# Optimization experiments

Measured on AMD Instinct MI355X. Metric: run time of the kernel, lower is better.

The kernel has to match this reference:

```python
import jax, jax.numpy as jnp
import numpy as np

HIDDEN = 150
EMBED = 300
OUT = 5
VOCAB = 100000
DEPTH = 13                      # complete binary tree
N = 2 ** DEPTH - 1              # 8191 nodes
L = 2 ** (DEPTH - 1)            # 4096 leaves
SCALE = 0.01


def _build_tree():
    # heap layout: node i internal iff i < N - L; children 2i+1, 2i+2
    words = np.full(N, -1, dtype=np.int64)
    rng = np.random.RandomState(0)
    words[N - L:] = rng.randint(0, VOCAB, size=L)
    lchs = np.zeros(N, dtype=np.int64)
    rchs = np.zeros(N, dtype=np.int64)
    internal = np.arange(N - L)
    lchs[internal] = 2 * internal + 1
    rchs[internal] = 2 * internal + 2
    scores = rng.randint(0, OUT, size=N).astype(np.int64)
    return scores, words, lchs, rchs


def setup_inputs() -> dict:
    key = jax.random.key(0)
    ks = jax.random.split(key, 24)
    p = lambda i, shp: jax.random.normal(ks[i], shp, dtype=jnp.float32) * SCALE
    scores, words, lchs, rchs = _build_tree()
    return {
        "Wi": p(0, (HIDDEN, EMBED)), "bi": p(1, (HIDDEN,)),
        "Wo": p(2, (HIDDEN, EMBED)), "bo": p(3, (HIDDEN,)),
        "Wu": p(4, (HIDDEN, EMBED)), "bu": p(5, (HIDDEN,)),
        "U0i": p(6, (HIDDEN, HIDDEN)), "U1i": p(7, (HIDDEN, HIDDEN)), "bbi": p(8, (HIDDEN,)),
        "U00f": p(9, (HIDDEN, HIDDEN)), "U01f": p(10, (HIDDEN, HIDDEN)),
        "U10f": p(11, (HIDDEN, HIDDEN)), "U11f": p(12, (HIDDEN, HIDDEN)), "bbf": p(13, (HIDDEN,)),
        "U0o": p(14, (HIDDEN, HIDDEN)), "U1o": p(15, (HIDDEN, HIDDEN)), "bbo": p(16, (HIDDEN,)),
        "U0u": p(17, (HIDDEN, HIDDEN)), "U1u": p(18, (HIDDEN, HIDDEN)), "bbu": p(19, (HIDDEN,)),
        "Why": p(20, (OUT, HIDDEN)), "by": p(21, (OUT,)),
        "word_embedding": jax.random.normal(ks[22], (VOCAB, EMBED), dtype=jnp.float32),
        "scores": jnp.asarray(scores), "words": jnp.asarray(words),
        "lchs": jnp.asarray(lchs), "rchs": jnp.asarray(rchs),
    }


def _tree_loss(Wi, bi, Wo, bo, Wu, bu, U0i, U1i, bbi, U00f, U01f, U10f, U11f,
               bbf, U0o, U1o, bbo, U0u, U1u, bbu, Why, by, word_embedding,
               scores, words, lchs, rchs):
    n = scores.shape[0]
    depth = int(np.log2(n + 1))
    leaf_start = 2 ** (depth - 1) - 1

    H_all = jnp.zeros((n, HIDDEN), dtype=Wi.dtype)
    C_all = jnp.zeros((n, HIDDEN), dtype=Wi.dtype)

    # leaf level (batched): cell = sigmoid(Wi e + bi) * tanh(Wu e + bu)
    emb = word_embedding[words[leaf_start:]]              # [L, 300]
    ig = jax.nn.sigmoid(emb @ Wi.T + bi)
    og = jax.nn.sigmoid(emb @ Wo.T + bo)
    uv = jnp.tanh(emb @ Wu.T + bu)
    c = ig * uv
    h = og * jnp.tanh(c)
    H_all = H_all.at[leaf_start:].set(h)
    C_all = C_all.at[leaf_start:].set(c)

    # internal levels, children-before-parents (level-wise batched Tree-LSTM)
    for d in range(depth - 2, -1, -1):
        s, e = 2 ** d - 1, 2 ** (d + 1) - 1
        li, ri = lchs[s:e], rchs[s:e]
        lh, rh = H_all[li], H_all[ri]
        lc, rc = C_all[li], C_all[ri]
        ig = jax.nn.sigmoid(lh @ U0i.T + rh @ U1i.T + bbi)
        fl = jax.nn.sigmoid(lh @ U00f.T + rh @ U01f.T + bbf)
        fr = jax.nn.sigmoid(lh @ U10f.T + rh @ U11f.T + bbf)
        og = jax.nn.sigmoid(lh @ U0o.T + rh @ U1o.T + bbo)
        uv = jnp.tanh(lh @ U0u.T + rh @ U1u.T + bbu)
        c = ig * uv + fl * lc + fr * rc
        h = og * jnp.tanh(c)
        H_all = H_all.at[s:e].set(h)
        C_all = C_all.at[s:e].set(c)

    # per-node NLL loss, summed over all nodes
    logits = H_all @ Why.T + by                            # [N, 5]
    logp = jax.nn.log_softmax(logits, axis=1)
    return -jnp.sum(logp[jnp.arange(n), scores])


def reference(Wi, bi, Wo, bo, Wu, bu, U0i, U1i, bbi, U00f, U01f, U10f, U11f,
              bbf, U0o, U1o, bbo, U0u, U1u, bbu, Why, by, word_embedding,
              scores, words, lchs, rchs):
    return _tree_loss(Wi, bi, Wo, bo, Wu, bu, U0i, U1i, bbi, U00f, U01f,
                      U10f, U11f, bbf, U0o, U1o, bbo, U0u, U1u, bbu, Why, by,
                      word_embedding, scores, words, lchs, rchs)
```

## Files before the change

kernel.cpp:

```cpp
#include <hip/hip_runtime.h>
#include <math.h>

#define HID 150
#define EMB 300
#define NOUT 5
#define NNODES 8191
#define NLEAF 4096
#define LEAF_START 4095
#define HSTR 152
#define UCOLS 768
#define WCOLS 452

constexpr int LOSS_BLOCKS = 64;

__device__ __forceinline__ float sigmoidf_(float x) { return 1.0f / (1.0f + __expf(-x)); }

__global__ __launch_bounds__(256) void prep_kernel(
    const float* __restrict__ Wi, const float* __restrict__ Wo, const float* __restrict__ Wu,
    const float* __restrict__ U0i, const float* __restrict__ U1i,
    const float* __restrict__ U00f, const float* __restrict__ U01f,
    const float* __restrict__ U10f, const float* __restrict__ U11f,
    const float* __restrict__ U0o, const float* __restrict__ U1o,
    const float* __restrict__ U0u, const float* __restrict__ U1u,
    float* __restrict__ Wt2, float* __restrict__ Ut3, float* __restrict__ Ut4)
{
    int idx = blockIdx.x * 256 + threadIdx.x;
    if (idx < EMB * WCOLS) {
        int e = idx / WCOLS, j = idx - e * WCOLS;
        float v = 0.f;
        if (j < 450) {
            const float* W; int h;
            if (j < 150)      { W = Wi; h = j; }
            else if (j < 300) { W = Wo; h = j - 150; }
            else              { W = Wu; h = j - 300; }
            v = W[h * EMB + e];
        }
        Wt2[idx] = v;
    }
    if (idx < EMB * UCOLS) {
        int e = idx / UCOLS, j = idx - e * UCOLS;
        const float* U0[5] = {U0i, U00f, U10f, U0o, U0u};
        const float* U1[5] = {U1i, U01f, U11f, U1o, U1u};
        {
            int hc = j >> 8, cw = j & 255;
            float v = 0.f;
            if (cw < 250) {
                int g = cw / 50, hp = cw - g * 50, h = hc * 50 + hp;
                v = (e < 150) ? U0[g][h * HID + e] : U1[g][h * HID + (e - 150)];
            }
            Ut3[idx] = v;
        }
        {
            int hc = j >> 7, cw = j & 127;
            float v = 0.f;
            if (cw < 125) {
                int g = cw / 25, hp = cw - g * 25, h = hc * 25 + hp;
                v = (e < 150) ? U0[g][h * HID + e] : U1[g][h * HID + (e - 150)];
            }
            Ut4[idx] = v;
        }
    }
}

__global__ __launch_bounds__(256) void leaf_v3(
    const float* __restrict__ Wt2,
    const float* __restrict__ bi, const float* __restrict__ bo, const float* __restrict__ bu,
    const float* __restrict__ emb, const int* __restrict__ words,
    float* __restrict__ H, float* __restrict__ C)
{
    constexpr int NB = 8;
    __shared__ __align__(16) float Xs[EMB * NB];
    __shared__ __align__(16) float Gs[2][NB][WCOLS];
    const int tid = threadIdx.x;
    const int leaf0 = LEAF_START + blockIdx.x * NB;

    for (int m = 0; m < NB; ++m) {
        const float* src = emb + (long)words[leaf0 + m] * EMB;
        for (int e = tid; e < EMB; e += 256) Xs[e * NB + m] = src[e];
    }
    __syncthreads();

    {
        const int half = tid >> 7;
        const int c = tid & 127;
        if (c < 113) {
            float acc[NB][4];
#pragma unroll
            for (int m = 0; m < NB; ++m)
#pragma unroll
                for (int q = 0; q < 4; ++q) acc[m][q] = 0.f;

            const int kbase = half * 150;
            const float* wp = Wt2 + (long)kbase * WCOLS + c * 4;
            const float* xp = Xs + kbase * NB;
#pragma unroll 4
            for (int k = 0; k < 150; ++k) {
                float4 w = *(const float4*)(wp + (long)k * WCOLS);
                float4 xa = *(const float4*)(xp + k * NB);
                float4 xb = *(const float4*)(xp + k * NB + 4);
                float x[NB] = {xa.x, xa.y, xa.z, xa.w, xb.x, xb.y, xb.z, xb.w};
#pragma unroll
                for (int m = 0; m < NB; ++m) {
                    acc[m][0] = fmaf(x[m], w.x, acc[m][0]);
                    acc[m][1] = fmaf(x[m], w.y, acc[m][1]);
                    acc[m][2] = fmaf(x[m], w.z, acc[m][2]);
                    acc[m][3] = fmaf(x[m], w.w, acc[m][3]);
                }
            }
#pragma unroll
            for (int m = 0; m < NB; ++m)
                *(float4*)&Gs[half][m][c * 4] = make_float4(acc[m][0], acc[m][1], acc[m][2], acc[m][3]);
        }
    }
    __syncthreads();

    for (int p = tid; p < NB * HID; p += 256) {
        int m = p / HID, h = p - m * HID;
        float gi = Gs[0][m][h]       + Gs[1][m][h];
        float go = Gs[0][m][150 + h] + Gs[1][m][150 + h];
        float gu = Gs[0][m][300 + h] + Gs[1][m][300 + h];
        float ig = sigmoidf_(gi + bi[h]);
        float og = sigmoidf_(go + bo[h]);
        float uv = tanhf(gu + bu[h]);
        float cc = ig * uv;
        float hh = og * tanhf(cc);
        long node = leaf0 + m;
        H[node * HSTR + h] = hh;
        C[node * HSTR + h] = cc;
    }
}

template<int NB>
__global__ __launch_bounds__(512) void level_h3(
    const float* __restrict__ Ut3,
    const float* __restrict__ bbi, const float* __restrict__ bbf,
    const float* __restrict__ bbo, const float* __restrict__ bbu,
    const int* __restrict__ lchs, const int* __restrict__ rchs,
    float* __restrict__ H, float* __restrict__ C, int s)
{
    __shared__ __align__(16) float Xs[EMB * NB];
    __shared__ __align__(16) float Gs[4][NB][256];
    __shared__ int lidx[NB], ridx[NB];
    const int tid = threadIdx.x;
    const int grp = blockIdx.x / 3, hc = blockIdx.x % 3;
    const int node0 = s + grp * NB;

    if (tid < NB) {
        lidx[tid] = lchs[node0 + tid];
        ridx[tid] = rchs[node0 + tid];
    }
    __syncthreads();

    for (int m = 0; m < NB; ++m) {
        const float* hl = H + (long)lidx[m] * HSTR;
        const float* hr = H + (long)ridx[m] * HSTR;
        for (int e = tid; e < EMB; e += 512)
            Xs[e * NB + m] = (e < HID) ? hl[e] : hr[e - HID];
    }
    __syncthreads();

    {
        const int kq = tid >> 7, c2 = tid & 127;
        float acc[NB][2];
#pragma unroll
        for (int m = 0; m < NB; ++m) { acc[m][0] = 0.f; acc[m][1] = 0.f; }

        const float* wp = Ut3 + (long)(kq * 75) * UCOLS + hc * 256 + 2 * c2;
        const float* xp = Xs + (kq * 75) * NB;
#pragma unroll 5
        for (int k = 0; k < 75; ++k) {
            float2 w = *(const float2*)(wp + (long)k * UCOLS);
            float x[NB];
            if constexpr (NB == 8) {
                float4 a = *(const float4*)(xp + k * 8);
                float4 b = *(const float4*)(xp + k * 8 + 4);
                x[0]=a.x; x[1]=a.y; x[2]=a.z; x[3]=a.w;
                x[4]=b.x; x[5]=b.y; x[6]=b.z; x[7]=b.w;
            } else if constexpr (NB == 4) {
                float4 a = *(const float4*)(xp + k * 4);
                x[0]=a.x; x[1]=a.y; x[2]=a.z; x[3]=a.w;
            } else if constexpr (NB == 2) {
                float2 a = *(const float2*)(xp + k * 2);
                x[0]=a.x; x[1]=a.y;
            } else {
                x[0] = xp[k];
            }
#pragma unroll
            for (int m = 0; m < NB; ++m) {
                acc[m][0] = fmaf(x[m], w.x, acc[m][0]);
                acc[m][1] = fmaf(x[m], w.y, acc[m][1]);
            }
        }
#pragma unroll
        for (int m = 0; m < NB; ++m)
            *(float2*)&Gs[kq][m][2 * c2] = make_float2(acc[m][0], acc[m][1]);
    }
    __syncthreads();

    for (int p = tid; p < NB * 50; p += 512) {
        int m = p / 50, hp = p - m * 50, h = hc * 50 + hp;
        float gi  = Gs[0][m][hp]       + Gs[1][m][hp]       + Gs[2][m][hp]       + Gs[3][m][hp];
        float gf0 = Gs[0][m][50 + hp]  + Gs[1][m][50 + hp]  + Gs[2][m][50 + hp]  + Gs[3][m][50 + hp];
        float gf1 = Gs[0][m][100 + hp] + Gs[1][m][100 + hp] + Gs[2][m][100 + hp] + Gs[3][m][100 + hp];
        float go  = Gs[0][m][150 + hp] + Gs[1][m][150 + hp] + Gs[2][m][150 + hp] + Gs[3][m][150 + hp];
        float gu  = Gs[0][m][200 + hp] + Gs[1][m][200 + hp] + Gs[2][m][200 + hp] + Gs[3][m][200 + hp];
        float ig = sigmoidf_(gi + bbi[h]);
        float fl = sigmoidf_(gf0 + bbf[h]);
        float fr = sigmoidf_(gf1 + bbf[h]);
        float og = sigmoidf_(go + bbo[h]);
        float uv = tanhf(gu + bbu[h]);
        float lc = C[(long)lidx[m] * HSTR + h];
        float rc = C[(long)ridx[m] * HSTR + h];
        float cc = ig * uv + fl * lc + fr * rc;
        float hh = og * tanhf(cc);
        long node = node0 + m;
        H[node * HSTR + h] = hh;
        C[node * HSTR + h] = cc;
    }
}

__global__ __launch_bounds__(512) void level_h6(
    const float* __restrict__ Ut4,
    const float* __restrict__ bbi, const float* __restrict__ bbf,
    const float* __restrict__ bbo, const float* __restrict__ bbu,
    const int* __restrict__ lchs, const int* __restrict__ rchs,
    float* __restrict__ H, float* __restrict__ C, int s)
{
    __shared__ __align__(16) float Xs[EMB];
    __shared__ __align__(16) float Gs[4][128];
    __shared__ int lr[2];
    const int tid = threadIdx.x;
    const int grp = blockIdx.x / 6, hc = blockIdx.x % 6;
    const int node = s + grp;

    if (tid < 2) lr[tid] = tid ? rchs[node] : lchs[node];
    __syncthreads();
    if (tid < EMB)
        Xs[tid] = (tid < HID) ? H[(long)lr[0] * HSTR + tid] : H[(long)lr[1] * HSTR + (tid - HID)];
    __syncthreads();

    {
        const int kq = tid >> 7, c = tid & 127;
        float acc = 0.f;
        const float* wp = Ut4 + (long)(kq * 75) * UCOLS + hc * 128 + c;
        const float* xp = Xs + kq * 75;
#pragma unroll 15
        for (int k = 0; k < 75; ++k)
            acc = fmaf(xp[k], wp[(long)k * UCOLS], acc);
        Gs[kq][c] = acc;
    }
    __syncthreads();

    if (tid < 25) {
        int hp = tid, h = hc * 25 + hp;
        float gi  = Gs[0][hp]       + Gs[1][hp]       + Gs[2][hp]       + Gs[3][hp];
        float gf0 = Gs[0][25 + hp]  + Gs[1][25 + hp]  + Gs[2][25 + hp]  + Gs[3][25 + hp];
        float gf1 = Gs[0][50 + hp]  + Gs[1][50 + hp]  + Gs[2][50 + hp]  + Gs[3][50 + hp];
        float go  = Gs[0][75 + hp]  + Gs[1][75 + hp]  + Gs[2][75 + hp]  + Gs[3][75 + hp];
        float gu  = Gs[0][100 + hp] + Gs[1][100 + hp] + Gs[2][100 + hp] + Gs[3][100 + hp];
        float ig = sigmoidf_(gi + bbi[h]);
        float fl = sigmoidf_(gf0 + bbf[h]);
        float fr = sigmoidf_(gf1 + bbf[h]);
        float og = sigmoidf_(go + bbo[h]);
        float uv = tanhf(gu + bbu[h]);
        float lc = C[(long)lr[0] * HSTR + h];
        float rc = C[(long)lr[1] * HSTR + h];
        float cc = ig * uv + fl * lc + fr * rc;
        float hh = og * tanhf(cc);
        H[(long)node * HSTR + h] = hh;
        C[(long)node * HSTR + h] = cc;
    }
}

__global__ __launch_bounds__(256) void loss_kernel(
    const float* __restrict__ H, const float* __restrict__ Why,
    const float* __restrict__ by, const int* __restrict__ scores,
    float* __restrict__ partials)
{
    __shared__ __align__(16) float Wys[NOUT][HSTR];
    __shared__ float bys[NOUT];
    __shared__ float red[256];
    int tid = threadIdx.x;
    for (int i = tid; i < NOUT * HID; i += 256) {
        int g = i / HID, k = i - g * HID;
        Wys[g][k] = Why[g * HID + k];
    }
    if (tid < NOUT) bys[tid] = by[tid];
    __syncthreads();

    float local = 0.f;
    for (int n = blockIdx.x * 256 + tid; n < NNODES; n += gridDim.x * 256) {
        const float* hr = H + (long)n * HSTR;
        float l0 = bys[0], l1 = bys[1], l2 = bys[2], l3 = bys[3], l4 = bys[4];
        for (int k = 0; k < 148; k += 4) {
            float4 hv = *(const float4*)(hr + k);
            float4 w0 = *(const float4*)&Wys[0][k];
            float4 w1 = *(const float4*)&Wys[1][k];
            float4 w2 = *(const float4*)&Wys[2][k];
            float4 w3 = *(const float4*)&Wys[3][k];
            float4 w4 = *(const float4*)&Wys[4][k];
            l0 += hv.x*w0.x + hv.y*w0.y + hv.z*w0.z + hv.w*w0.w;
            l1 += hv.x*w1.x + hv.y*w1.y + hv.z*w1.z + hv.w*w1.w;
            l2 += hv.x*w2.x + hv.y*w2.y + hv.z*w2.z + hv.w*w2.w;
            l3 += hv.x*w3.x + hv.y*w3.y + hv.z*w3.z + hv.w*w3.w;
            l4 += hv.x*w4.x + hv.y*w4.y + hv.z*w4.z + hv.w*w4.w;
        }
        for (int k = 148; k < HID; ++k) {
            float hv = hr[k];
            l0 += hv * Wys[0][k]; l1 += hv * Wys[1][k]; l2 += hv * Wys[2][k];
            l3 += hv * Wys[3][k]; l4 += hv * Wys[4][k];
        }
        float mx = fmaxf(fmaxf(fmaxf(l0, l1), fmaxf(l2, l3)), l4);
        float se = __expf(l0 - mx) + __expf(l1 - mx) + __expf(l2 - mx) +
                   __expf(l3 - mx) + __expf(l4 - mx);
        float lse = mx + __logf(se);
        int sc = scores[n];
        float lsc = (sc == 0) ? l0 : (sc == 1) ? l1 : (sc == 2) ? l2 : (sc == 3) ? l3 : l4;
        local += lse - lsc;
    }
    red[tid] = local;
    __syncthreads();
    for (int st = 128; st > 0; st >>= 1) {
        if (tid < st) red[tid] += red[tid + st];
        __syncthreads();
    }
    if (tid == 0) partials[blockIdx.x] = red[0];
}

__global__ void loss_final(const float* __restrict__ partials, float* __restrict__ out, int nparts)
{
    if (threadIdx.x == 0 && blockIdx.x == 0) {
        float s = 0.f;
        for (int i = 0; i < nparts; ++i) s += partials[i];
        out[0] = s;
    }
}

extern "C" void kernel_launch(void* const* d_in, const int* in_sizes, int n_in,
                              void* d_out, int out_size, void* d_ws, size_t ws_size,
                              hipStream_t stream)
{
    const float* Wi   = (const float*)d_in[0];
    const float* bi   = (const float*)d_in[1];
    const float* Wo   = (const float*)d_in[2];
    const float* bo   = (const float*)d_in[3];
    const float* Wu   = (const float*)d_in[4];
    const float* bu   = (const float*)d_in[5];
    const float* U0i  = (const float*)d_in[6];
    const float* U1i  = (const float*)d_in[7];
    const float* bbi  = (const float*)d_in[8];
    const float* U00f = (const float*)d_in[9];
    const float* U01f = (const float*)d_in[10];
    const float* U10f = (const float*)d_in[11];
    const float* U11f = (const float*)d_in[12];
    const float* bbf  = (const float*)d_in[13];
    const float* U0o  = (const float*)d_in[14];
    const float* U1o  = (const float*)d_in[15];
    const float* bbo  = (const float*)d_in[16];
    const float* U0u  = (const float*)d_in[17];
    const float* U1u  = (const float*)d_in[18];
    const float* bbu  = (const float*)d_in[19];
    const float* Why  = (const float*)d_in[20];
    const float* by   = (const float*)d_in[21];
    const float* emb  = (const float*)d_in[22];
    const int* scores = (const int*)d_in[23];
    const int* words  = (const int*)d_in[24];
    const int* lchs   = (const int*)d_in[25];
    const int* rchs   = (const int*)d_in[26];

    float* ws = (float*)d_ws;
    float* Wt2 = ws;
    float* Ut3 = Wt2 + EMB * WCOLS;
    float* Ut4 = Ut3 + EMB * UCOLS;
    float* H   = Ut4 + EMB * UCOLS;
    float* C   = H + (long)NNODES * HSTR;
    float* partials = C + (long)NNODES * HSTR;
    float* out = (float*)d_out;

    hipLaunchKernelGGL(prep_kernel, dim3(900), dim3(256), 0, stream,
                       Wi, Wo, Wu, U0i, U1i, U00f, U01f, U10f, U11f,
                       U0o, U1o, U0u, U1u, Wt2, Ut3, Ut4);

    hipLaunchKernelGGL(leaf_v3, dim3(NLEAF / 8), dim3(256), 0, stream,
                       Wt2, bi, bo, bu, emb, words, H, C);

    for (int d = 11; d >= 0; --d) {
        int s = (1 << d) - 1, count = 1 << d;
        if (d >= 10) {
            hipLaunchKernelGGL(HIP_KERNEL_NAME(level_h3<8>), dim3((count / 8) * 3), dim3(512), 0, stream,
                               Ut3, bbi, bbf, bbo, bbu, lchs, rchs, H, C, s);
        } else if (d == 9) {
            hipLaunchKernelGGL(HIP_KERNEL_NAME(level_h3<4>), dim3((count / 4) * 3), dim3(512), 0, stream,
                               Ut3, bbi, bbf, bbo, bbu, lchs, rchs, H, C, s);
        } else if (d == 8) {
            hipLaunchKernelGGL(HIP_KERNEL_NAME(level_h3<2>), dim3((count / 2) * 3), dim3(512), 0, stream,
                               Ut3, bbi, bbf, bbo, bbu, lchs, rchs, H, C, s);
        } else if (d == 7) {
            hipLaunchKernelGGL(HIP_KERNEL_NAME(level_h3<1>), dim3(count * 3), dim3(512), 0, stream,
                               Ut3, bbi, bbf, bbo, bbu, lchs, rchs, H, C, s);
        } else {
            hipLaunchKernelGGL(level_h6, dim3(count * 6), dim3(512), 0, stream,
                               Ut4, bbi, bbf, bbo, bbu, lchs, rchs, H, C, s);
        }
    }

    hipLaunchKernelGGL(loss_kernel, dim3(LOSS_BLOCKS), dim3(256), 0, stream,
                       H, Why, by, scores, partials);
    hipLaunchKernelGGL(loss_final, dim3(1), dim3(64), 0, stream,
                       partials, out, LOSS_BLOCKS);
}
```

Measured before the change: 369.8 us.

## Batch more nodes per block in leaf and wide tree levels

The leaf kernel now processes 16 leaves per 512-thread block, and a new level kernel handles 16 nodes per block for the two widest internal levels. Smaller levels shift to larger per-block node batches, and the gather of child states and embeddings is flattened across all threads. The aim is more reuse of each weight load across nodes, cutting weight traffic per node, at the cost of fewer blocks, more registers and more shared memory per block, which can reduce occupancy on the narrower levels.

```diff
diff --git a/kernel.cpp b/kernel.cpp
--- a/kernel.cpp
+++ b/kernel.cpp
@@ -62,59 +62,62 @@
     }
 }
 
-__global__ __launch_bounds__(256) void leaf_v3(
+__global__ __launch_bounds__(512) void leaf_v4(
     const float* __restrict__ Wt2,
     const float* __restrict__ bi, const float* __restrict__ bo, const float* __restrict__ bu,
     const float* __restrict__ emb, const int* __restrict__ words,
     float* __restrict__ H, float* __restrict__ C)
 {
-    constexpr int NB = 8;
+    constexpr int NB = 16;
     __shared__ __align__(16) float Xs[EMB * NB];
     __shared__ __align__(16) float Gs[2][NB][WCOLS];
+    __shared__ int wq[NB];
     const int tid = threadIdx.x;
     const int leaf0 = LEAF_START + blockIdx.x * NB;
 
-    for (int m = 0; m < NB; ++m) {
-        const float* src = emb + (long)words[leaf0 + m] * EMB;
-        for (int e = tid; e < EMB; e += 256) Xs[e * NB + m] = src[e];
+    if (tid < NB) wq[tid] = words[leaf0 + tid];
+    __syncthreads();
+
+    for (int p = tid; p < NB * EMB; p += 512) {
+        int m = p / EMB, e = p - m * EMB;
+        Xs[e * NB + m] = emb[(long)wq[m] * EMB + e];
     }
     __syncthreads();
 
     {
-        const int half = tid >> 7;
-        const int c = tid & 127;
-        if (c < 113) {
-            float acc[NB][4];
-#pragma unroll
-            for (int m = 0; m < NB; ++m)
-#pragma unroll
-                for (int q = 0; q < 4; ++q) acc[m][q] = 0.f;
-
-            const int kbase = half * 150;
-            const float* wp = Wt2 + (long)kbase * WCOLS + c * 4;
+        const int kq = tid >> 8;
+        const int c = tid & 255;
+        if (c < 226) {
+            float acc[NB][2];
+#pragma unroll
+            for (int m = 0; m < NB; ++m) { acc[m][0] = 0.f; acc[m][1] = 0.f; }
+
+            const int kbase = kq * 150;
+            const float* wp = Wt2 + (long)kbase * WCOLS + 2 * c;
             const float* xp = Xs + kbase * NB;
-#pragma unroll 4
+#pragma unroll 2
             for (int k = 0; k < 150; ++k) {
-                float4 w = *(const float4*)(wp + (long)k * WCOLS);
-                float4 xa = *(const float4*)(xp + k * NB);
-                float4 xb = *(const float4*)(xp + k * NB + 4);
-                float x[NB] = {xa.x, xa.y, xa.z, xa.w, xb.x, xb.y, xb.z, xb.w};
+                float2 w = *(const float2*)(wp + (long)k * WCOLS);
+                float4 a0 = *(const float4*)(xp + k * NB);
+                float4 a1 = *(const float4*)(xp + k * NB + 4);
+                float4 a2 = *(const float4*)(xp + k * NB + 8);
+                float4 a3 = *(const float4*)(xp + k * NB + 12);
+                float x[NB] = {a0.x, a0.y, a0.z, a0.w, a1.x, a1.y, a1.z, a1.w,
+                               a2.x, a2.y, a2.z, a2.w, a3.x, a3.y, a3.z, a3.w};
 #pragma unroll
                 for (int m = 0; m < NB; ++m) {
                     acc[m][0] = fmaf(x[m], w.x, acc[m][0]);
                     acc[m][1] = fmaf(x[m], w.y, acc[m][1]);
-                    acc[m][2] = fmaf(x[m], w.z, acc[m][2]);
-                    acc[m][3] = fmaf(x[m], w.w, acc[m][3]);
                 }
             }
 #pragma unroll
             for (int m = 0; m < NB; ++m)
-                *(float4*)&Gs[half][m][c * 4] = make_float4(acc[m][0], acc[m][1], acc[m][2], acc[m][3]);
-        }
-    }
-    __syncthreads();
-
-    for (int p = tid; p < NB * HID; p += 256) {
+                *(float2*)&Gs[kq][m][2 * c] = make_float2(acc[m][0], acc[m][1]);
+        }
+    }
+    __syncthreads();
+
+    for (int p = tid; p < NB * HID; p += 512) {
         int m = p / HID, h = p - m * HID;
         float gi = Gs[0][m][h]       + Gs[1][m][h];
         float go = Gs[0][m][150 + h] + Gs[1][m][150 + h];
@@ -130,6 +133,81 @@
     }
 }
 
+__global__ __launch_bounds__(512) void level_h3w(
+    const float* __restrict__ Ut3,
+    const float* __restrict__ bbi, const float* __restrict__ bbf,
+    const float* __restrict__ bbo, const float* __restrict__ bbu,
+    const int* __restrict__ lchs, const int* __restrict__ rchs,
+    float* __restrict__ H, float* __restrict__ C, int s)
+{
+    constexpr int NB = 16;
+    __shared__ __align__(16) float Xs[EMB * NB];
+    __shared__ __align__(16) float Gs[2][NB][256];
+    __shared__ int lidx[NB], ridx[NB];
+    const int tid = threadIdx.x;
+    const int grp = blockIdx.x / 3, hc = blockIdx.x % 3;
+    const int node0 = s + grp * NB;
+
+    if (tid < NB) {
+        lidx[tid] = lchs[node0 + tid];
+        ridx[tid] = rchs[node0 + tid];
+    }
+    __syncthreads();
+
+    for (int p = tid; p < NB * EMB; p += 512) {
+        int m = p / EMB, e = p - m * EMB;
+        Xs[e * NB + m] = (e < HID) ? H[(long)lidx[m] * HSTR + e]
+                                   : H[(long)ridx[m] * HSTR + (e - HID)];
+    }
+    __syncthreads();
+
+    {
+        const int kq = tid >> 8, c = tid & 255;
+        float acc[NB];
+#pragma unroll
+        for (int m = 0; m < NB; ++m) acc[m] = 0.f;
+
+        const float* wp = Ut3 + (long)(kq * 150) * UCOLS + hc * 256 + c;
+        const float* xp = Xs + (kq * 150) * NB;
+#pragma unroll 2
+        for (int k = 0; k < 150; ++k) {
+            float w = wp[(long)k * UCOLS];
+            float4 a0 = *(const float4*)(xp + k * NB);
+            float4 a1 = *(const float4*)(xp + k * NB + 4);
+            float4 a2 = *(const float4*)(xp + k * NB + 8);
+            float4 a3 = *(const float4*)(xp + k * NB + 12);
+            float x[NB] = {a0.x, a0.y, a0.z, a0.w, a1.x, a1.y, a1.z, a1.w,
+                           a2.x, a2.y, a2.z, a2.w, a3.x, a3.y, a3.z, a3.w};
+#pragma unroll
+            for (int m = 0; m < NB; ++m) acc[m] = fmaf(x[m], w, acc[m]);
+        }
+#pragma unroll
+        for (int m = 0; m < NB; ++m) Gs[kq][m][c] = acc[m];
+    }
+    __syncthreads();
+
+    for (int p = tid; p < NB * 50; p += 512) {
+        int m = p / 50, hp = p - m * 50, h = hc * 50 + hp;
+        float gi  = Gs[0][m][hp]       + Gs[1][m][hp];
+        float gf0 = Gs[0][m][50 + hp]  + Gs[1][m][50 + hp];
+        float gf1 = Gs[0][m][100 + hp] + Gs[1][m][100 + hp];
+        float go  = Gs[0][m][150 + hp] + Gs[1][m][150 + hp];
+        float gu  = Gs[0][m][200 + hp] + Gs[1][m][200 + hp];
+        float ig = sigmoidf_(gi + bbi[h]);
+        float fl = sigmoidf_(gf0 + bbf[h]);
+        float fr = sigmoidf_(gf1 + bbf[h]);
+        float og = sigmoidf_(go + bbo[h]);
+        float uv = tanhf(gu + bbu[h]);
+        float lc = C[(long)lidx[m] * HSTR + h];
+        float rc = C[(long)ridx[m] * HSTR + h];
+        float cc = ig * uv + fl * lc + fr * rc;
+        float hh = og * tanhf(cc);
+        long node = node0 + m;
+        H[node * HSTR + h] = hh;
+        C[node * HSTR + h] = cc;
+    }
+}
+
 template<int NB>
 __global__ __launch_bounds__(512) void level_h3(
     const float* __restrict__ Ut3,
@@ -151,11 +229,10 @@
     }
     __syncthreads();
 
-    for (int m = 0; m < NB; ++m) {
-        const float* hl = H + (long)lidx[m] * HSTR;
-        const float* hr = H + (long)ridx[m] * HSTR;
-        for (int e = tid; e < EMB; e += 512)
-            Xs[e * NB + m] = (e < HID) ? hl[e] : hr[e - HID];
+    for (int p = tid; p < NB * EMB; p += 512) {
+        int m = p / EMB, e = p - m * EMB;
+        Xs[e * NB + m] = (e < HID) ? H[(long)lidx[m] * HSTR + e]
+                                   : H[(long)ridx[m] * HSTR + (e - HID)];
     }
     __syncthreads();
 
@@ -381,22 +458,22 @@
                        Wi, Wo, Wu, U0i, U1i, U00f, U01f, U10f, U11f,
                        U0o, U1o, U0u, U1u, Wt2, Ut3, Ut4);
 
-    hipLaunchKernelGGL(leaf_v3, dim3(NLEAF / 8), dim3(256), 0, stream,
+    hipLaunchKernelGGL(leaf_v4, dim3(NLEAF / 16), dim3(512), 0, stream,
                        Wt2, bi, bo, bu, emb, words, H, C);
 
     for (int d = 11; d >= 0; --d) {
         int s = (1 << d) - 1, count = 1 << d;
         if (d >= 10) {
+            hipLaunchKernelGGL(level_h3w, dim3((count / 16) * 3), dim3(512), 0, stream,
+                               Ut3, bbi, bbf, bbo, bbu, lchs, rchs, H, C, s);
+        } else if (d == 9) {
             hipLaunchKernelGGL(HIP_KERNEL_NAME(level_h3<8>), dim3((count / 8) * 3), dim3(512), 0, stream,
                                Ut3, bbi, bbf, bbo, bbu, lchs, rchs, H, C, s);
-        } else if (d == 9) {
+        } else if (d == 8) {
             hipLaunchKernelGGL(HIP_KERNEL_NAME(level_h3<4>), dim3((count / 4) * 3), dim3(512), 0, stream,
                                Ut3, bbi, bbf, bbo, bbu, lchs, rchs, H, C, s);
-        } else if (d == 8) {
+        } else if (d == 7) {
             hipLaunchKernelGGL(HIP_KERNEL_NAME(level_h3<2>), dim3((count / 2) * 3), dim3(512), 0, stream,
-                               Ut3, bbi, bbf, bbo, bbu, lchs, rchs, H, C, s);
-        } else if (d == 7) {
-            hipLaunchKernelGGL(HIP_KERNEL_NAME(level_h3<1>), dim3(count * 3), dim3(512), 0, stream,
                                Ut3, bbi, bbf, bbo, bbu, lchs, rchs, H, C, s);
         } else {
             hipLaunchKernelGGL(level_h6, dim3(count * 6), dim3(512), 0, stream,
```

New measurement: 370.8 us, median of 2. About the same (+0.3%).
